# Kernel optimization log

Measured on AMD Instinct MI355X. Metric: run time of the kernel, lower is better.

## Reference

```python
import jax, jax.numpy as jnp
import numpy as np

EPS = 1e-05
B, M, N, P = 32, 1024, 1024, 256


def _xavier(key, shape):
    fan_in, fan_out = shape[0], shape[1]
    limit = np.sqrt(6.0 / (fan_in + fan_out))
    return jax.random.uniform(key, shape, jnp.float32, -limit, limit)


def setup_inputs() -> dict:
    key = jax.random.key(0)
    ks = jax.random.split(key, 6)
    return {
        "x": jax.random.normal(ks[0], (B, M, N), jnp.float32),
        "original_xj_y": _xavier(ks[1], (N, P)),
        "original_xi_y": _xavier(ks[2], (M, P)),
        "permuted_xj_y": _xavier(ks[3], (M, P)),
        "permuted_xi_y": _xavier(ks[4], (N, P)),
        "gamma_o_sum": jnp.ones((P,), jnp.float32),
        "gamma_o": jnp.ones((P, P), jnp.float32),
        "gamma_p_sum": jnp.ones((P,), jnp.float32),
        "gamma_p": jnp.ones((P, P), jnp.float32),
        "gamma": jnp.ones((P, P), jnp.float32),
        "beta_o_sum": jnp.zeros((P,), jnp.float32),
        "beta_o": jnp.zeros((P, P), jnp.float32),
        "beta_p_sum": jnp.zeros((P,), jnp.float32),
        "beta_p": jnp.zeros((P, P), jnp.float32),
        "beta": jnp.zeros((P, P), jnp.float32),
    }


def _normalize(x, axes, gamma, beta):
    mean = jnp.mean(x, axis=axes, keepdims=True)
    std = jnp.sqrt(jnp.var(x, axis=axes, keepdims=True, ddof=1))  # torch std is unbiased
    return gamma * ((x - mean) / (std + EPS)) + beta


def reference(x, original_xj_y, original_xi_y, permuted_xj_y, permuted_xi_y,
              gamma_o_sum, gamma_o, gamma_p_sum, gamma_p, gamma,
              beta_o_sum, beta_o, beta_p_sum, beta_p, beta):
    permuted = jnp.swapaxes(x, -1, -2)  # [B, N, M]

    # original path
    oyy = x @ original_xj_y                      # [B, M, P]
    o_sum = _normalize(oyy.sum(axis=-2), (-1,), gamma_o_sum, beta_o_sum) + 1.0  # [B, P]
    oyy = jnp.swapaxes(oyy, -1, -2) @ original_xi_y  # [B, P, P]
    oyy = jnp.swapaxes(oyy, -1, -2)
    oyy = _normalize(oyy, (-2, -1), gamma_o, beta_o)

    # permuted path
    pyy = permuted @ permuted_xj_y               # [B, N, P]
    p_sum = _normalize(pyy.sum(axis=-2), (-1,), gamma_p_sum, beta_p_sum) + 1.0  # [B, P]
    pyy = jnp.swapaxes(pyy, -1, -2) @ permuted_xi_y  # [B, P, P]
    pyy = jnp.swapaxes(pyy, -1, -2)
    pyy = _normalize(pyy, (-2, -1), gamma_p, beta_p)

    relations = jnp.einsum('ij,ik->ijk', o_sum, p_sum)  # [B, P, P]
    projected = (oyy * relations) @ (pyy * relations)   # [B, P, P]
    projected = _normalize(projected, (-2, -1), gamma, beta)
    return (projected, relations)
```

## Files before the change

### kernel.cpp

```cpp
#include <hip/hip_runtime.h>
#include <hip/hip_bf16.h>

#define PP 256
#define BB 32
#define MM 1024
#define NN 1024

constexpr float EPSF = 1e-5f;

typedef __attribute__((ext_vector_type(8))) short short8v;
typedef __attribute__((ext_vector_type(4))) short short4v;
typedef __attribute__((ext_vector_type(4))) float f32x4;

__device__ inline float bf2f(short s) {
  union { unsigned u; float f; } cv;
  cv.u = ((unsigned)(unsigned short)s) << 16;
  return cv.f;
}
__device__ inline short f2bf(float f) {
  union { float f; unsigned u; } cv; cv.f = f;
  unsigned u = cv.u;
  unsigned r = (u + 0x7fffu + ((u >> 16) & 1u)) >> 16;
  return (short)r;
}

__device__ inline void gload16(const void* g, void* l) {
  __builtin_amdgcn_global_load_lds(
      (const __attribute__((address_space(1))) unsigned*)g,
      (__attribute__((address_space(3))) unsigned*)l, 16, 0, 0);
}

__global__ __launch_bounds__(256)
void wconv4(const float* __restrict__ s0, const float* __restrict__ s1,
            const float* __restrict__ s2, const float* __restrict__ s3,
            short* __restrict__ d0, short* __restrict__ d1,
            short* __restrict__ d2, short* __restrict__ d3)
{
  const float* src = (blockIdx.z == 0) ? s0 : (blockIdx.z == 1) ? s1
                    : (blockIdx.z == 2) ? s2 : s3;
  short* dst = (blockIdx.z == 0) ? d0 : (blockIdx.z == 1) ? d1
              : (blockIdx.z == 2) ? d2 : d3;
  __shared__ float tile[64][65];
  const int c0 = blockIdx.x * 64, r0 = blockIdx.y * 64;
  const int tid = threadIdx.x;
#pragma unroll
  for (int i = 0; i < 16; ++i) {
    int idx = i * 256 + tid;
    int r = idx >> 6, c = idx & 63;
    tile[r][c] = src[(long)(r0 + r) * 256 + (c0 + c)];
  }
  __syncthreads();
#pragma unroll
  for (int i = 0; i < 16; ++i) {
    int idx = i * 256 + tid;
    int rr = idx >> 6, cc = idx & 63;
    dst[(long)(c0 + rr) * 1024 + (r0 + cc)] = f2bf(tile[cc][rr]);
  }
}

__global__ __launch_bounds__(256)
void tr2_f32(const float* __restrict__ s0, const float* __restrict__ s1,
             float* __restrict__ d0, float* __restrict__ d1)
{
  const float* src = blockIdx.z ? s1 : s0;
  float* dst = blockIdx.z ? d1 : d0;
  __shared__ float tile[64][65];
  const int c0 = blockIdx.x * 64, r0 = blockIdx.y * 64;
  const int tid = threadIdx.x;
#pragma unroll
  for (int i = 0; i < 16; ++i) {
    int idx = i * 256 + tid;
    int r = idx >> 6, c = idx & 63;
    tile[r][c] = src[(long)(r0 + r) * 256 + (c0 + c)];
  }
  __syncthreads();
#pragma unroll
  for (int i = 0; i < 16; ++i) {
    int idx = i * 256 + tid;
    int rr = idx >> 6, cc = idx & 63;
    dst[(long)(c0 + rr) * 256 + (r0 + cc)] = tile[cc][rr];
  }
}

__global__ __launch_bounds__(256)
void gemm_xcat(const float* __restrict__ x, const short* __restrict__ wcat,
               short* __restrict__ oyyT, short* __restrict__ UT,
               float* __restrict__ rowsum)
{
  constexpr int BM = 128, BN = 128;
  __shared__ short As[4 * BM * 8];
  __shared__ short Bs[4 * BN * 8];

  const int b = blockIdx.z;
  const float* Ab = x + (long)b * MM * NN;
  const int m0 = blockIdx.x * BM;
  const int n0 = blockIdx.y * BN;

  const int tid = threadIdx.x;
  const int l = tid & 63, w = tid >> 6;
  const int wr = w >> 1, wc = w & 1;
  const int lk = l >> 4, lr = l & 15;
  const int sm = tid >> 2, skc = tid & 3;

  f32x4 acc[4][4];
#pragma unroll
  for (int fm = 0; fm < 4; ++fm)
#pragma unroll
    for (int fn = 0; fn < 4; ++fn)
      acc[fm][fn] = (f32x4){0.f, 0.f, 0.f, 0.f};

  float rs0 = 0.f, rs1 = 0.f;
  const bool doRs = (blockIdx.y == 0);

  for (int k0 = 0; k0 < NN; k0 += 32) {
#pragma unroll
    for (int i = 0; i < 2; ++i) {
      const int m = i * 64 + sm;
      const float* src = Ab + (long)(m0 + m) * NN + k0 + skc * 8;
      float4 v0 = *reinterpret_cast<const float4*>(src);
      float4 v1 = *reinterpret_cast<const float4*>(src + 4);
      if (doRs) {
        float t = v0.x + v0.y + v0.z + v0.w + v1.x + v1.y + v1.z + v1.w;
        if (i == 0) rs0 += t; else rs1 += t;
      }
      short8v pk;
      pk[0] = f2bf(v0.x); pk[1] = f2bf(v0.y); pk[2] = f2bf(v0.z); pk[3] = f2bf(v0.w);
      pk[4] = f2bf(v1.x); pk[5] = f2bf(v1.y); pk[6] = f2bf(v1.z); pk[7] = f2bf(v1.w);
      const int idx = ((skc * BM + m) * 8) ^ (skc << 4);
      *reinterpret_cast<short8v*>(&As[idx]) = pk;
    }
#pragma unroll
    for (int i = 0; i < 2; ++i) {
      const int s = i * 256 + tid;
      const int kc = s >> 7, n = s & 127;
      gload16(wcat + (long)(n0 + n) * NN + k0 + kc * 8, &Bs[s * 8]);
    }
    __syncthreads();

    short8v af[4], bf[4];
#pragma unroll
    for (int fm = 0; fm < 4; ++fm) {
      const int row = wr * 64 + fm * 16 + lr;
      af[fm] = *reinterpret_cast<const short8v*>(&As[((lk * BM + row) * 8) ^ (lk << 4)]);
    }
#pragma unroll
    for (int fn = 0; fn < 4; ++fn)
      bf[fn] = *reinterpret_cast<const short8v*>(&Bs[(lk * BN + wc * 64 + fn * 16 + lr) * 8]);
#pragma unroll
    for (int fm = 0; fm < 4; ++fm)
#pragma unroll
      for (int fn = 0; fn < 4; ++fn)
        acc[fm][fn] = __builtin_amdgcn_mfma_f32_16x16x32_bf16(
            af[fm], bf[fn], acc[fm][fn], 0, 0, 0);
    __syncthreads();
  }

  if (doRs) {
    rs0 += __shfl_xor(rs0, 1); rs0 += __shfl_xor(rs0, 2);
    rs1 += __shfl_xor(rs1, 1); rs1 += __shfl_xor(rs1, 2);
    if ((tid & 3) == 0) {
      rowsum[(long)b * MM + m0 + sm] = rs0;
      rowsum[(long)b * MM + m0 + 64 + sm] = rs1;
    }
  }

  short* Cb = ((n0 < 256) ? oyyT : UT) + (long)b * PP * MM;
  const int nb = n0 & 255;
#pragma unroll
  for (int fm = 0; fm < 4; ++fm)
#pragma unroll
    for (int fn = 0; fn < 4; ++fn) {
      const int c = nb + wc * 64 + fn * 16 + lr;
      const int rb = m0 + wr * 64 + fm * 16 + lk * 4;
      short4v pk;
#pragma unroll
      for (int j = 0; j < 4; ++j) pk[j] = f2bf(acc[fm][fn][j]);
      *reinterpret_cast<short4v*>(&Cb[(long)c * MM + rb]) = pk;
    }
}

__global__ __launch_bounds__(256)
void gemm_dual(const short* __restrict__ oyyT, const short* __restrict__ wo2T,
               const short* __restrict__ UT, const short* __restrict__ wp1T,
               float* __restrict__ t2T, float* __restrict__ p2)
{
  constexpr int BM = 64, BN = 64;
  __shared__ short As[4 * BM * 8];
  __shared__ short Bs[4 * BN * 8];

  const int z = blockIdx.z;
  const short* Ab; const short* Bb; float* Cb;
  if (z < 32) { Ab = oyyT + (long)z * PP * MM; Bb = wo2T; Cb = t2T + ((long)z << 16); }
  else { Ab = UT + (long)(z - 32) * PP * MM; Bb = wp1T; Cb = p2 + ((long)(z - 32) << 16); }

  const int m0 = blockIdx.x * BM, n0 = blockIdx.y * BN;
  const int tid = threadIdx.x;
  const int l = tid & 63, w = tid >> 6;
  const int wr = w >> 1, wc = w & 1;
  const int lk = l >> 4, lr = l & 15;

  f32x4 acc[2][2];
#pragma unroll
  for (int fm = 0; fm < 2; ++fm)
#pragma unroll
    for (int fn = 0; fn < 2; ++fn)
      acc[fm][fn] = (f32x4){0.f, 0.f, 0.f, 0.f};

  for (int k0 = 0; k0 < MM; k0 += 32) {
    {
      const int kc = tid >> 6, m = tid & 63;
      gload16(Ab + (long)(m0 + m) * MM + k0 + kc * 8, &As[tid * 8]);
      gload16(Bb + (long)(n0 + m) * MM + k0 + kc * 8, &Bs[tid * 8]);
    }
    __syncthreads();
    short8v af[2], bf[2];
#pragma unroll
    for (int fm = 0; fm < 2; ++fm)
      af[fm] = *(const short8v*)&As[(lk * BM + wr * 32 + fm * 16 + lr) * 8];
#pragma unroll
    for (int fn = 0; fn < 2; ++fn)
      bf[fn] = *(const short8v*)&Bs[(lk * BN + wc * 32 + fn * 16 + lr) * 8];
#pragma unroll
    for (int fm = 0; fm < 2; ++fm)
#pragma unroll
      for (int fn = 0; fn < 2; ++fn)
        acc[fm][fn] = __builtin_amdgcn_mfma_f32_16x16x32_bf16(
            af[fm], bf[fn], acc[fm][fn], 0, 0, 0);
    __syncthreads();
  }

#pragma unroll
  for (int fm = 0; fm < 2; ++fm)
#pragma unroll
    for (int fn = 0; fn < 2; ++fn) {
      const int c = n0 + wc * 32 + fn * 16 + lr;
      const int rb = m0 + wr * 32 + fm * 16 + lk * 4;
      *(f32x4*)&Cb[(long)c * PP + rb] = acc[fm][fn];
    }
}

__global__ __launch_bounds__(256)
void gemm_pp(const short* __restrict__ A, const short* __restrict__ BT,
             float* __restrict__ C)
{
  constexpr int BM = 64, BN = 64;
  __shared__ short As[4 * BM * 8];
  __shared__ short Bs[4 * BN * 8];
  const int b = blockIdx.z;
  const short* Ab = A + ((long)b << 16);
  const short* Bb = BT + ((long)b << 16);
  float* Cb = C + ((long)b << 16);
  const int m0 = blockIdx.x * BM, n0 = blockIdx.y * BN;
  const int tid = threadIdx.x;
  const int l = tid & 63, w = tid >> 6;
  const int wr = w >> 1, wc = w & 1;
  const int lk = l >> 4, lr = l & 15;

  f32x4 acc[2][2];
#pragma unroll
  for (int fm = 0; fm < 2; ++fm)
#pragma unroll
    for (int fn = 0; fn < 2; ++fn)
      acc[fm][fn] = (f32x4){0.f, 0.f, 0.f, 0.f};

  for (int k0 = 0; k0 < PP; k0 += 32) {
    {
      const int kc = tid >> 6, m = tid & 63;
      gload16(Ab + (long)(m0 + m) * PP + k0 + kc * 8, &As[tid * 8]);
      gload16(Bb + (long)(n0 + m) * PP + k0 + kc * 8, &Bs[tid * 8]);
    }
    __syncthreads();
    short8v af[2], bf[2];
#pragma unroll
    for (int fm = 0; fm < 2; ++fm)
      af[fm] = *(const short8v*)&As[(lk * BM + wr * 32 + fm * 16 + lr) * 8];
#pragma unroll
    for (int fn = 0; fn < 2; ++fn)
      bf[fn] = *(const short8v*)&Bs[(lk * BN + wc * 32 + fn * 16 + lr) * 8];
#pragma unroll
    for (int fm = 0; fm < 2; ++fm)
#pragma unroll
      for (int fn = 0; fn < 2; ++fn)
        acc[fm][fn] = __builtin_amdgcn_mfma_f32_16x16x32_bf16(
            af[fm], bf[fn], acc[fm][fn], 0, 0, 0);
    __syncthreads();
  }

#pragma unroll
  for (int fm = 0; fm < 2; ++fm)
#pragma unroll
    for (int fn = 0; fn < 2; ++fn) {
      const int c = n0 + wc * 32 + fn * 16 + lr;
      const int rb = m0 + wr * 32 + fm * 16 + lk * 4;
#pragma unroll
      for (int j = 0; j < 4; ++j)
        Cb[(long)(rb + j) * PP + c] = acc[fm][fn][j];
    }
}

__global__ __launch_bounds__(256)
void colsum_bf16(const short* __restrict__ srcT, float* __restrict__ raw)
{
  const int b = blockIdx.y;
  const int w = threadIdx.x >> 6, l = threadIdx.x & 63;
  const int p = blockIdx.x * 4 + w;
  const short* row = srcT + ((long)b * 256 + p) * 1024;
  short8v v1 = *(const short8v*)&row[l * 8];
  short8v v2 = *(const short8v*)&row[(64 + l) * 8];
  float s = 0.f;
#pragma unroll
  for (int j = 0; j < 8; ++j) s += bf2f(v1[j]) + bf2f(v2[j]);
#pragma unroll
  for (int off = 32; off; off >>= 1) s += __shfl_down(s, off);
  if (l == 0) raw[(long)b * 256 + p] = s;
}

__global__ __launch_bounds__(256)
void psum_dot(const short* __restrict__ wp1T, const float* __restrict__ rowsum,
              float* __restrict__ rawP)
{
  __shared__ float rsm[1024];
  const int b = blockIdx.x;
  for (int i = threadIdx.x; i < 1024; i += 256) rsm[i] = rowsum[(long)b * 1024 + i];
  __syncthreads();
  const int p = threadIdx.x;
  const short* wrow = wp1T + (long)p * 1024;
  float s = 0.f;
  for (int k = 0; k < 1024; k += 8) {
    short8v v = *(const short8v*)&wrow[k];
#pragma unroll
    for (int j = 0; j < 8; ++j) s = fmaf(bf2f(v[j]), rsm[k + j], s);
  }
  rawP[(long)b * 256 + p] = s;
}

__device__ inline void block_reduce2(float& v1, float& v2, float* red)
{
#pragma unroll
  for (int off = 32; off > 0; off >>= 1) {
    v1 += __shfl_down(v1, off);
    v2 += __shfl_down(v2, off);
  }
  const int lane = threadIdx.x & 63, wid = threadIdx.x >> 6;
  if (lane == 0) { red[wid * 2] = v1; red[wid * 2 + 1] = v2; }
  __syncthreads();
  v1 = red[0] + red[2] + red[4] + red[6];
  v2 = red[1] + red[3] + red[5] + red[7];
}

__global__ __launch_bounds__(256)
void norm_sum2(const float* __restrict__ raw2,
               const float* __restrict__ g_os, const float* __restrict__ b_os,
               const float* __restrict__ g_ps, const float* __restrict__ b_ps,
               float* __restrict__ o_sum, float* __restrict__ p_sum)
{
  const int bb = blockIdx.x;
  const bool isP = bb >= 32;
  const int b = bb & 31;
  const float* raw = raw2 + (isP ? 8192 : 0);
  const float* gamma = isP ? g_ps : g_os;
  const float* beta = isP ? b_ps : b_os;
  float* outp = isP ? p_sum : o_sum;
  const int p = threadIdx.x;
  float s = raw[(long)b * 256 + p];
  __shared__ float red[8];
  float v1 = s, v2 = s * s;
  block_reduce2(v1, v2, red);
  const float mean = v1 / 256.0f;
  float var = fmaxf((v2 - v1 * mean) / 255.0f, 0.f);
  const float inv = 1.0f / (sqrtf(var) + EPSF);
  outp[(long)b * 256 + p] = gamma[p] * (s - mean) * inv + beta[p] + 1.0f;
}

__global__ __launch_bounds__(256)
void stats_dual(const float* __restrict__ t2T, const float* __restrict__ p2,
                float* __restrict__ part)
{
  const int y = blockIdx.y, chunk = blockIdx.x;
  const float* s = (y < 32 ? t2T + ((long)y << 16)
                           : p2 + ((long)(y - 32) << 16)) + (long)chunk * 8192;
  float v1 = 0.f, v2 = 0.f;
  for (int i = threadIdx.x; i < 2048; i += 256) {
    float4 xv = *reinterpret_cast<const float4*>(&s[i * 4]);
    v1 += xv.x + xv.y + xv.z + xv.w;
    v2 = fmaf(xv.x, xv.x, fmaf(xv.y, xv.y, fmaf(xv.z, xv.z, fmaf(xv.w, xv.w, v2))));
  }
  __shared__ float red[8];
  block_reduce2(v1, v2, red);
  if (threadIdx.x == 0) {
    part[(y * 8 + chunk) * 2] = v1;
    part[(y * 8 + chunk) * 2 + 1] = v2;
  }
}

__global__ void stats_fin2(const float* __restrict__ part,
                           float* __restrict__ stO, float* __restrict__ stP)
{
  const int t = threadIdx.x;
  const int y = t;
  float v1 = 0.f, v2 = 0.f;
#pragma unroll
  for (int c = 0; c < 8; ++c) {
    v1 += part[(y * 8 + c) * 2];
    v2 += part[(y * 8 + c) * 2 + 1];
  }
  const float mean = v1 / 65536.0f;
  const float var = fmaxf((v2 - v1 * mean) / 65535.0f, 0.f);
  float* st = (t < 32) ? stO : stP;
  st[(t & 31) * 2] = mean;
  st[(t & 31) * 2 + 1] = 1.0f / (sqrtf(var) + EPSF);
}

__global__ __launch_bounds__(256)
void stats_part(const float* __restrict__ src, float* __restrict__ part)
{
  const int b = blockIdx.y, chunk = blockIdx.x;
  const float* s = src + ((long)b << 16) + (long)chunk * 8192;
  float v1 = 0.f, v2 = 0.f;
  for (int i = threadIdx.x; i < 2048; i += 256) {
    float4 xv = *reinterpret_cast<const float4*>(&s[i * 4]);
    v1 += xv.x + xv.y + xv.z + xv.w;
    v2 = fmaf(xv.x, xv.x, fmaf(xv.y, xv.y, fmaf(xv.z, xv.z, fmaf(xv.w, xv.w, v2))));
  }
  __shared__ float red[8];
  block_reduce2(v1, v2, red);
  if (threadIdx.x == 0) {
    part[(b * 8 + chunk) * 2] = v1;
    part[(b * 8 + chunk) * 2 + 1] = v2;
  }
}

__global__ void stats_fin(const float* __restrict__ part, float* __restrict__ st)
{
  const int b = threadIdx.x;
  if (b < 32) {
    float v1 = 0.f, v2 = 0.f;
#pragma unroll
    for (int c = 0; c < 8; ++c) {
      v1 += part[(b * 8 + c) * 2];
      v2 += part[(b * 8 + c) * 2 + 1];
    }
    const float mean = v1 / 65536.0f;
    const float var = fmaxf((v2 - v1 * mean) / 65535.0f, 0.f);
    st[b * 2] = mean;
    st[b * 2 + 1] = 1.0f / (sqrtf(var) + EPSF);
  }
}

__global__ __launch_bounds__(256)
void prep2(const float* __restrict__ t2T, const float* __restrict__ p2,
           const float* __restrict__ o_sum, const float* __restrict__ p_sum,
           const float* __restrict__ gamma_o, const float* __restrict__ beta_o,
           const float* __restrict__ gTp, const float* __restrict__ bTp,
           const float* __restrict__ stO, const float* __restrict__ stP,
           short* __restrict__ Ap, short* __restrict__ BpT,
           float* __restrict__ out)
{
  const long idx = (long)blockIdx.x * 256 + threadIdx.x;
  const int b = (int)(idx >> 16);
  const int rc = (int)(idx & 65535);
  const int r = rc >> 8, c = rc & 255;
  const float mO = stO[b * 2], iO = stO[b * 2 + 1];
  const float mP = stP[b * 2], iP = stP[b * 2 + 1];
  const float relA = o_sum[(b << 8) + r] * p_sum[(b << 8) + c];
  const float on = gamma_o[rc] * (t2T[idx] - mO) * iO + beta_o[rc];
  Ap[idx] = f2bf(on * relA);
  const float pn = gTp[rc] * (p2[idx] - mP) * iP + bTp[rc];
  BpT[idx] = f2bf(pn * o_sum[(b << 8) + c] * p_sum[(b << 8) + r]);
  out[(long)BB * 65536 + idx] = relA;
}

__global__ __launch_bounds__(256)
void final_half(const float* __restrict__ proj, const float* __restrict__ stF,
                const float* __restrict__ gamma, const float* __restrict__ beta,
                float* __restrict__ out)
{
  const long idx = (long)blockIdx.x * 256 + threadIdx.x;
  const int b = (int)(idx >> 16);
  const int ij = (int)(idx & 65535);
  out[idx] = gamma[ij] * (proj[idx] - stF[b * 2]) * stF[b * 2 + 1] + beta[ij];
}

extern "C" void kernel_launch(void* const* d_in, const int* in_sizes, int n_in,
                              void* d_out, int out_size, void* d_ws, size_t ws_size,
                              hipStream_t stream)
{
  const float* x    = (const float*)d_in[0];
  const float* Wo1  = (const float*)d_in[1];
  const float* Wo2  = (const float*)d_in[2];
  const float* Wp1  = (const float*)d_in[3];
  const float* Wp2  = (const float*)d_in[4];
  const float* g_os = (const float*)d_in[5];
  const float* g_o  = (const float*)d_in[6];
  const float* g_ps = (const float*)d_in[7];
  const float* g_p  = (const float*)d_in[8];
  const float* g    = (const float*)d_in[9];
  const float* b_os = (const float*)d_in[10];
  const float* b_o  = (const float*)d_in[11];
  const float* b_ps = (const float*)d_in[12];
  const float* b_p  = (const float*)d_in[13];
  const float* b_   = (const float*)d_in[14];
  float* out = (float*)d_out;

  short* wcat = (short*)d_ws;
  short* wo2T = wcat + 524288;
  short* wp1T = wo2T + 262144;
  short* oyyT = wp1T + 262144;
  short* UT   = oyyT + 8388608;
  float* gTp  = (float*)(UT + 8388608);
  float* bTp  = gTp + 65536;
  float* rowsumX = bTp + 65536;
  float* t2T  = rowsumX + 32768;
  float* p2   = t2T + 2097152;
  float* proj = p2 + 2097152;
  short* Ap   = (short*)(proj + 2097152);
  short* BpT  = Ap + 2097152;
  float* raw2 = (float*)(BpT + 2097152);
  float* o_sum = raw2 + 16384;
  float* p_sum = o_sum + 8192;
  float* part  = p_sum + 8192;
  float* partF = part + 1024;
  float* stO   = partF + 512;
  float* stP   = stO + 64;
  float* stF   = stP + 64;

  wconv4<<<dim3(4, 16, 4), 256, 0, stream>>>(Wo1, Wo2, Wp1, Wp2,
                                             wcat, wo2T, wp1T, wcat + 262144);
  tr2_f32<<<dim3(4, 4, 2), 256, 0, stream>>>(g_p, b_p, gTp, bTp);

  gemm_xcat<<<dim3(8, 4, 32), 256, 0, stream>>>(x, wcat, oyyT, UT, rowsumX);

  colsum_bf16<<<dim3(64, 32), 256, 0, stream>>>(oyyT, raw2);
  psum_dot<<<32, 256, 0, stream>>>(wp1T, rowsumX, raw2 + 8192);
  norm_sum2<<<64, 256, 0, stream>>>(raw2, g_os, b_os, g_ps, b_ps, o_sum, p_sum);

  gemm_dual<<<dim3(4, 4, 64), 256, 0, stream>>>(oyyT, wo2T, UT, wp1T, t2T, p2);

  stats_dual<<<dim3(8, 64), 256, 0, stream>>>(t2T, p2, part);
  stats_fin2<<<1, 64, 0, stream>>>(part, stO, stP);

  prep2<<<8192, 256, 0, stream>>>(t2T, p2, o_sum, p_sum, g_o, b_o, gTp, bTp,
                                  stO, stP, Ap, BpT, out);

  gemm_pp<<<dim3(4, 4, 32), 256, 0, stream>>>(Ap, BpT, proj);

  stats_part<<<dim3(8, 32), 256, 0, stream>>>(proj, partF);
  stats_fin<<<1, 64, 0, stream>>>(partF, stF);

  final_half<<<8192, 256, 0, stream>>>(proj, stF, g, b_, out);
}
```

Before: 194.7 us.

## Double-buffer LDS tiles and prefetch next K-slice in GEMM kernels

```diff
diff --git a/kernel.cpp b/kernel.cpp
--- a/kernel.cpp
+++ b/kernel.cpp
@@ -82,14 +82,14 @@
   }
 }
 
-__global__ __launch_bounds__(256)
+__global__ __launch_bounds__(256, 4)
 void gemm_xcat(const float* __restrict__ x, const short* __restrict__ wcat,
                short* __restrict__ oyyT, short* __restrict__ UT,
                float* __restrict__ rowsum)
 {
   constexpr int BM = 128, BN = 128;
-  __shared__ short As[4 * BM * 8];
-  __shared__ short Bs[4 * BN * 8];
+  __shared__ short As[2][4 * BM * 8];
+  __shared__ short Bs[2][4 * BN * 8];
 
   const int b = blockIdx.z;
   const float* Ab = x + (long)b * MM * NN;
@@ -102,6 +102,14 @@
   const int lk = l >> 4, lr = l & 15;
   const int sm = tid >> 2, skc = tid & 3;
 
+  const float* aptr0 = Ab + (long)(m0 + sm) * NN + skc * 8;
+  const float* aptr1 = Ab + (long)(m0 + 64 + sm) * NN + skc * 8;
+  const int bn = tid & 127, bk0 = (tid >> 7) * 8;
+  const short* bptr = wcat + (long)(n0 + bn) * NN + bk0;
+
+  const int sA0 = ((skc * BM + sm) * 8) ^ (skc << 4);
+  const int sA1 = ((skc * BM + 64 + sm) * 8) ^ (skc << 4);
+
   f32x4 acc[4][4];
 #pragma unroll
   for (int fm = 0; fm < 4; ++fm)
@@ -111,47 +119,62 @@
 
   float rs0 = 0.f, rs1 = 0.f;
   const bool doRs = (blockIdx.y == 0);
-
-  for (int k0 = 0; k0 < NN; k0 += 32) {
-#pragma unroll
-    for (int i = 0; i < 2; ++i) {
-      const int m = i * 64 + sm;
-      const float* src = Ab + (long)(m0 + m) * NN + k0 + skc * 8;
-      float4 v0 = *reinterpret_cast<const float4*>(src);
-      float4 v1 = *reinterpret_cast<const float4*>(src + 4);
-      if (doRs) {
-        float t = v0.x + v0.y + v0.z + v0.w + v1.x + v1.y + v1.z + v1.w;
-        if (i == 0) rs0 += t; else rs1 += t;
-      }
-      short8v pk;
-      pk[0] = f2bf(v0.x); pk[1] = f2bf(v0.y); pk[2] = f2bf(v0.z); pk[3] = f2bf(v0.w);
-      pk[4] = f2bf(v1.x); pk[5] = f2bf(v1.y); pk[6] = f2bf(v1.z); pk[7] = f2bf(v1.w);
-      const int idx = ((skc * BM + m) * 8) ^ (skc << 4);
-      *reinterpret_cast<short8v*>(&As[idx]) = pk;
-    }
-#pragma unroll
-    for (int i = 0; i < 2; ++i) {
-      const int s = i * 256 + tid;
-      const int kc = s >> 7, n = s & 127;
-      gload16(wcat + (long)(n0 + n) * NN + k0 + kc * 8, &Bs[s * 8]);
-    }
-    __syncthreads();
-
+  float4 a00, a01, a10, a11;
+
+#define XCAT_LOAD_A(k0_) do { \
+    a00 = *reinterpret_cast<const float4*>(aptr0 + (k0_)); \
+    a01 = *reinterpret_cast<const float4*>(aptr0 + (k0_) + 4); \
+    a10 = *reinterpret_cast<const float4*>(aptr1 + (k0_)); \
+    a11 = *reinterpret_cast<const float4*>(aptr1 + (k0_) + 4); \
+  } while (0)
+
+#define XCAT_STAGE_B(buf_, k0_) do { \
+    gload16(bptr + (k0_), &Bs[buf_][tid * 8]); \
+    gload16(bptr + (k0_) + 16, &Bs[buf_][(tid + 256) * 8]); \
+  } while (0)
+
+#define XCAT_STAGE_A(buf_) do { \
+    if (doRs) { \
+      rs0 += a00.x + a00.y + a00.z + a00.w + a01.x + a01.y + a01.z + a01.w; \
+      rs1 += a10.x + a10.y + a10.z + a10.w + a11.x + a11.y + a11.z + a11.w; \
+    } \
+    short8v pk0, pk1; \
+    pk0[0] = f2bf(a00.x); pk0[1] = f2bf(a00.y); pk0[2] = f2bf(a00.z); pk0[3] = f2bf(a00.w); \
+    pk0[4] = f2bf(a01.x); pk0[5] = f2bf(a01.y); pk0[6] = f2bf(a01.z); pk0[7] = f2bf(a01.w); \
+    pk1[0] = f2bf(a10.x); pk1[1] = f2bf(a10.y); pk1[2] = f2bf(a10.z); pk1[3] = f2bf(a10.w); \
+    pk1[4] = f2bf(a11.x); pk1[5] = f2bf(a11.y); pk1[6] = f2bf(a11.z); pk1[7] = f2bf(a11.w); \
+    *reinterpret_cast<short8v*>(&As[buf_][sA0]) = pk0; \
+    *reinterpret_cast<short8v*>(&As[buf_][sA1]) = pk1; \
+  } while (0)
+
+  XCAT_LOAD_A(0);
+  XCAT_STAGE_B(0, 0);
+  XCAT_STAGE_A(0);
+  __syncthreads();
+
+  for (int kt = 0; kt < 32; ++kt) {
+    const int cur = kt & 1, nxt = cur ^ 1;
+    if (kt < 31) {
+      const int k1 = (kt + 1) * 32;
+      XCAT_LOAD_A(k1);
+      XCAT_STAGE_B(nxt, k1);
+    }
     short8v af[4], bf[4];
 #pragma unroll
     for (int fm = 0; fm < 4; ++fm) {
       const int row = wr * 64 + fm * 16 + lr;
-      af[fm] = *reinterpret_cast<const short8v*>(&As[((lk * BM + row) * 8) ^ (lk << 4)]);
+      af[fm] = *reinterpret_cast<const short8v*>(&As[cur][((lk * BM + row) * 8) ^ (lk << 4)]);
     }
 #pragma unroll
     for (int fn = 0; fn < 4; ++fn)
-      bf[fn] = *reinterpret_cast<const short8v*>(&Bs[(lk * BN + wc * 64 + fn * 16 + lr) * 8]);
+      bf[fn] = *reinterpret_cast<const short8v*>(&Bs[cur][(lk * BN + wc * 64 + fn * 16 + lr) * 8]);
 #pragma unroll
     for (int fm = 0; fm < 4; ++fm)
 #pragma unroll
       for (int fn = 0; fn < 4; ++fn)
         acc[fm][fn] = __builtin_amdgcn_mfma_f32_16x16x32_bf16(
             af[fm], bf[fn], acc[fm][fn], 0, 0, 0);
+    if (kt < 31) XCAT_STAGE_A(nxt);
     __syncthreads();
   }
 
@@ -185,8 +208,8 @@
                float* __restrict__ t2T, float* __restrict__ p2)
 {
   constexpr int BM = 64, BN = 64;
-  __shared__ short As[4 * BM * 8];
-  __shared__ short Bs[4 * BN * 8];
+  __shared__ short As[2][4 * BM * 8];
+  __shared__ short Bs[2][4 * BN * 8];
 
   const int z = blockIdx.z;
   const short* Ab; const short* Bb; float* Cb;
@@ -198,6 +221,9 @@
   const int l = tid & 63, w = tid >> 6;
   const int wr = w >> 1, wc = w & 1;
   const int lk = l >> 4, lr = l & 15;
+  const int kc = tid >> 6, mloc = tid & 63;
+  const short* aP = Ab + (long)(m0 + mloc) * MM + kc * 8;
+  const short* bP = Bb + (long)(n0 + mloc) * MM + kc * 8;
 
   f32x4 acc[2][2];
 #pragma unroll
@@ -206,20 +232,23 @@
     for (int fn = 0; fn < 2; ++fn)
       acc[fm][fn] = (f32x4){0.f, 0.f, 0.f, 0.f};
 
-  for (int k0 = 0; k0 < MM; k0 += 32) {
-    {
-      const int kc = tid >> 6, m = tid & 63;
-      gload16(Ab + (long)(m0 + m) * MM + k0 + kc * 8, &As[tid * 8]);
-      gload16(Bb + (long)(n0 + m) * MM + k0 + kc * 8, &Bs[tid * 8]);
-    }
-    __syncthreads();
+  gload16(aP, &As[0][tid * 8]);
+  gload16(bP, &Bs[0][tid * 8]);
+  __syncthreads();
+
+  for (int kt = 0; kt < 32; ++kt) {
+    const int cur = kt & 1, nxt = cur ^ 1;
+    if (kt < 31) {
+      gload16(aP + (kt + 1) * 32, &As[nxt][tid * 8]);
+      gload16(bP + (kt + 1) * 32, &Bs[nxt][tid * 8]);
+    }
     short8v af[2], bf[2];
 #pragma unroll
     for (int fm = 0; fm < 2; ++fm)
-      af[fm] = *(const short8v*)&As[(lk * BM + wr * 32 + fm * 16 + lr) * 8];
+      af[fm] = *(const short8v*)&As[cur][(lk * BM + wr * 32 + fm * 16 + lr) * 8];
 #pragma unroll
     for (int fn = 0; fn < 2; ++fn)
-      bf[fn] = *(const short8v*)&Bs[(lk * BN + wc * 32 + fn * 16 + lr) * 8];
+      bf[fn] = *(const short8v*)&Bs[cur][(lk * BN + wc * 32 + fn * 16 + lr) * 8];
 #pragma unroll
     for (int fm = 0; fm < 2; ++fm)
 #pragma unroll
@@ -244,8 +273,8 @@
              float* __restrict__ C)
 {
   constexpr int BM = 64, BN = 64;
-  __shared__ short As[4 * BM * 8];
-  __shared__ short Bs[4 * BN * 8];
+  __shared__ short As[2][4 * BM * 8];
+  __shared__ short Bs[2][4 * BN * 8];
   const int b = blockIdx.z;
   const short* Ab = A + ((long)b << 16);
   const short* Bb = BT + ((long)b << 16);
@@ -255,6 +284,9 @@
   const int l = tid & 63, w = tid >> 6;
   const int wr = w >> 1, wc = w & 1;
   const int lk = l >> 4, lr = l & 15;
+  const int kc = tid >> 6, mloc = tid & 63;
+  const short* aP = Ab + (long)(m0 + mloc) * PP + kc * 8;
+  const short* bP = Bb + (long)(n0 + mloc) * PP + kc * 8;
 
   f32x4 acc[2][2];
 #pragma unroll
@@ -263,20 +295,23 @@
     for (int fn = 0; fn < 2; ++fn)
       acc[fm][fn] = (f32x4){0.f, 0.f, 0.f, 0.f};
 
-  for (int k0 = 0; k0 < PP; k0 += 32) {
-    {
-      const int kc = tid >> 6, m = tid & 63;
-      gload16(Ab + (long)(m0 + m) * PP + k0 + kc * 8, &As[tid * 8]);
-      gload16(Bb + (long)(n0 + m) * PP + k0 + kc * 8, &Bs[tid * 8]);
-    }
-    __syncthreads();
+  gload16(aP, &As[0][tid * 8]);
+  gload16(bP, &Bs[0][tid * 8]);
+  __syncthreads();
+
+  for (int kt = 0; kt < 8; ++kt) {
+    const int cur = kt & 1, nxt = cur ^ 1;
+    if (kt < 7) {
+      gload16(aP + (kt + 1) * 32, &As[nxt][tid * 8]);
+      gload16(bP + (kt + 1) * 32, &Bs[nxt][tid * 8]);
+    }
     short8v af[2], bf[2];
 #pragma unroll
     for (int fm = 0; fm < 2; ++fm)
-      af[fm] = *(const short8v*)&As[(lk * BM + wr * 32 + fm * 16 + lr) * 8];
+      af[fm] = *(const short8v*)&As[cur][(lk * BM + wr * 32 + fm * 16 + lr) * 8];
 #pragma unroll
     for (int fn = 0; fn < 2; ++fn)
-      bf[fn] = *(const short8v*)&Bs[(lk * BN + wc * 32 + fn * 16 + lr) * 8];
+      bf[fn] = *(const short8v*)&Bs[cur][(lk * BN + wc * 32 + fn * 16 + lr) * 8];
 #pragma unroll
     for (int fm = 0; fm < 2; ++fm)
 #pragma unroll
@@ -397,12 +432,11 @@
                            float* __restrict__ stO, float* __restrict__ stP)
 {
   const int t = threadIdx.x;
-  const int y = t;
   float v1 = 0.f, v2 = 0.f;
 #pragma unroll
   for (int c = 0; c < 8; ++c) {
-    v1 += part[(y * 8 + c) * 2];
-    v2 += part[(y * 8 + c) * 2 + 1];
+    v1 += part[(t * 8 + c) * 2];
+    v2 += part[(t * 8 + c) * 2 + 1];
   }
   const float mean = v1 / 65536.0f;
   const float var = fmaxf((v2 - v1 * mean) / 65535.0f, 0.f);
```

Result: faster. 168.9 us (-13.2%).
